# Kernel tuning notes

Hardware: AMD Instinct MI355X
Metric: run time of the kernel (lower is better)

Reference implementation:

```python
import jax, jax.numpy as jnp
import numpy as np
from jax import lax

B, NODE, T, D_IN = 8, 1024, 12, 16
HID, GAT_OUT, PRED_LEN = 32, 32, 6
HEADS = 3
F_IN = HID * T      # 384
C = GAT_OUT * T     # 384
N = B * NODE        # 8192
E = 65536


def setup_inputs() -> dict:
    key = jax.random.key(0)
    ks = jax.random.split(key, 24)
    s = 0.05
    inp = {}
    inp["x"] = jax.random.normal(ks[0], (B, NODE, T, D_IN), jnp.float32)
    inp["edge_index"] = jax.random.randint(ks[1], (2, E), 0, N)
    inp["edge_attr"] = jax.random.normal(ks[2], (E, 1), jnp.float32)
    inp["batch_vec"] = jnp.repeat(jnp.arange(B), NODE)
    inp["alpha"] = 1.0
    # GRU params (torch gate order: r, z, n)
    inp["Wih"] = jax.random.normal(ks[3], (3 * HID, D_IN), jnp.float32) * s
    inp["Whh"] = jax.random.normal(ks[4], (3 * HID, HID), jnp.float32) * s
    inp["bih"] = jax.random.normal(ks[5], (3 * HID,), jnp.float32) * s
    inp["bhh"] = jax.random.normal(ks[6], (3 * HID,), jnp.float32) * s
    # GATConv params
    inp["Wgat"] = jax.random.normal(ks[7], (HEADS * C, F_IN), jnp.float32) * s
    inp["att_src"] = jax.random.normal(ks[8], (1, HEADS, C), jnp.float32) * s
    inp["att_dst"] = jax.random.normal(ks[9], (1, HEADS, C), jnp.float32) * s
    inp["Wedge"] = jax.random.normal(ks[10], (HEADS * C, 1), jnp.float32) * s
    inp["att_edge"] = jax.random.normal(ks[11], (1, HEADS, C), jnp.float32) * s
    inp["gat_bias"] = jax.random.normal(ks[12], (C,), jnp.float32) * s
    # predictors / classifiers
    inp["Wp1"] = jax.random.normal(ks[13], (1, GAT_OUT), jnp.float32) * s
    inp["bp1"] = jax.random.normal(ks[14], (1,), jnp.float32) * s
    inp["Wp3"] = jax.random.normal(ks[15], (PRED_LEN, T), jnp.float32) * s
    inp["bp3"] = jax.random.normal(ks[16], (PRED_LEN,), jnp.float32) * s
    inp["Wc1"] = jax.random.normal(ks[17], (GAT_OUT, T * GAT_OUT), jnp.float32) * s
    inp["bc1"] = jax.random.normal(ks[18], (GAT_OUT,), jnp.float32) * s
    inp["Wc2"] = jax.random.normal(ks[19], (2, GAT_OUT), jnp.float32) * s
    inp["bc2"] = jax.random.normal(ks[20], (2,), jnp.float32) * s
    return inp


def _gru(x, Wih, Whh, bih, bhh):
    # x: [rows, T, D_IN] -> [rows, T, HID]
    h0 = jnp.zeros((x.shape[0], HID), x.dtype)

    def step(h, xt):
        gi = xt @ Wih.T + bih
        gh = h @ Whh.T + bhh
        ir, iz, inn = jnp.split(gi, 3, axis=-1)
        hr, hz, hn = jnp.split(gh, 3, axis=-1)
        r = jax.nn.sigmoid(ir + hr)
        z = jax.nn.sigmoid(iz + hz)
        n = jnp.tanh(inn + r * hn)
        h_new = (1.0 - z) * n + z * h
        return h_new, h_new

    _, hs = lax.scan(step, h0, jnp.swapaxes(x, 0, 1))
    return jnp.swapaxes(hs, 0, 1)


def _gat(x, edge_index, edge_attr, Wgat, att_src, att_dst, Wedge, att_edge, bias):
    # PyG GATConv, heads=HEADS, concat=False, edge_dim=1, no self loops
    h = (x @ Wgat.T).reshape(N, HEADS, C)          # [N,H,C]
    a_src = (h * att_src).sum(-1)                  # [N,H]
    a_dst = (h * att_dst).sum(-1)                  # [N,H]
    src, dst = edge_index[0], edge_index[1]
    e = (edge_attr @ Wedge.T).reshape(-1, HEADS, C)
    a_edge = (e * att_edge).sum(-1)                # [E,H]
    a = jax.nn.leaky_relu(a_src[src] + a_dst[dst] + a_edge, 0.2)
    amax = jax.ops.segment_max(a, dst, num_segments=N)
    a = jnp.exp(a - amax[dst])
    denom = jax.ops.segment_sum(a, dst, num_segments=N)
    a = a / (denom[dst] + 1e-16)                   # segment softmax over incoming edges
    msg = h[src] * a[:, :, None]                   # [E,H,C]
    out = jax.ops.segment_sum(msg, dst, num_segments=N)
    return out.mean(axis=1) + bias                 # concat=False -> head mean


def reference(x, edge_index, edge_attr, batch_vec, alpha,
              Wih, Whh, bih, bhh,
              Wgat, att_src, att_dst, Wedge, att_edge, gat_bias,
              Wp1, bp1, Wp3, bp3, Wc1, bc1, Wc2, bc2):
    gru_in = x.reshape(-1, T, D_IN)                       # [N,T,D]
    gru_out = _gru(gru_in, Wih, Whh, bih, bhh)            # [N,T,HID]
    gat_in = gru_out.reshape(N, F_IN)
    gat_out = _gat(gat_in, edge_index, edge_attr, Wgat, att_src, att_dst,
                   Wedge, att_edge, gat_bias)             # [N,C]
    lin_in = gat_out.reshape(-1, T, GAT_OUT)              # [N,T,GAT_OUT]
    p = jax.nn.relu(jnp.einsum('ntc,oc->nto', lin_in, Wp1) + bp1).squeeze(-1)  # [N,T]
    p = jax.nn.relu(p @ Wp3.T + bp3)                      # [N,PRED_LEN]
    out_pred = p.reshape(B, NODE, PRED_LEN)
    # GRL is identity in forward
    pooled = jax.ops.segment_max(gat_out, batch_vec, num_segments=B)  # [B,C]
    l1 = pooled @ Wc1.T + bc1
    l2 = l1 @ Wc2.T + bc2
    out_label = jax.nn.softmax(l2, axis=1)
    return out_pred, out_label
```

## Files before the change

kernel.cpp:

```cpp
#include <hip/hip_runtime.h>
#include <hip/hip_bf16.h>

#define N_NODES 8192
#define E_EDGES 65536
#define HEADS 3
#define CDIM 384
#define NHC 1152
#define T_STEPS 12
#define D_IN 16
#define HID 32
#define PRED_LEN 6
#define OUT_LABEL_OFF 49152

#define O_X        0u
#define O_WIH      1572864u
#define O_WHH      1574400u
#define O_BIH      1577472u
#define O_BHH      1577568u
#define O_WGAT     1577664u
#define O_ATTS     2020032u
#define O_ATTD     2021184u
#define O_WEDGE    2022336u
#define O_ATTE     2023488u
#define O_GBIAS    2024640u
#define O_WP1      2025024u
#define O_BP1      2025056u
#define O_WP3      2025057u
#define O_BP3      2025129u
#define O_WC1      2025135u
#define O_BC1      2037423u
#define O_WC2      2037455u
#define O_BC2      2037519u
#define O_EATTR    2037521u
#define CONV_TOTAL 2103057u

#define O_GATIN    2103072u
#define O_GATB     O_GATIN
#define O_WGATB    (O_GATIN + 1572864u)
#define O_DEG      (O_GATIN + 1794048u)
#define O_ROWST    (O_GATIN + 1802240u)
#define O_CURS     (O_GATIN + 1810432u)
#define O_CSRE     (O_GATIN + 1818624u)
#define O_HFEAT    5248800u
#define O_ASRC     14685984u
#define O_ADST     14710560u
#define O_ARAW     14735136u
#define O_WEXP     14931744u
#define O_AMAX     15128352u
#define O_DENOM    15152928u
#define O_GMEAN    15177504u
#define O_POOLED   18323232u
#define O_KH       18326304u
#define O_FLAG     18326307u

typedef __attribute__((ext_vector_type(8))) short short8;
typedef __attribute__((ext_vector_type(4))) float floatx4;

__device__ __forceinline__ float b2f(unsigned short u) {
    return __uint_as_float(((unsigned)u) << 16);
}
__device__ __forceinline__ unsigned short f2b(float f) {
    __hip_bfloat16 b = __float2bfloat16(f);
    return *(unsigned short*)&b;
}
__device__ __forceinline__ short f2bs(float f) {
    __hip_bfloat16 b = __float2bfloat16(f);
    return *(short*)&b;
}
__device__ __forceinline__ unsigned enc_f(float f) {
    unsigned u = __float_as_uint(f);
    return (u & 0x80000000u) ? ~u : (u | 0x80000000u);
}
__device__ __forceinline__ float dec_f(unsigned e) {
    return __uint_as_float((e & 0x80000000u) ? (e & 0x7FFFFFFFu) : ~e);
}
__device__ __forceinline__ float fast_rcp(float x) {
    return __builtin_amdgcn_rcpf(x);
}

__global__ __launch_bounds__(256) void fill_detect(
    const unsigned short* __restrict__ wih_raw,
    int* __restrict__ flag,
    float* __restrict__ W)
{
    if (blockIdx.x == 0 && threadIdx.x < 64) {
        int lane = threadIdx.x;
        int cnt = 0;
#pragma unroll
        for (int i = 0; i < 8; i++) {
            unsigned short h = wih_raw[(lane * 8 + i) * 2];
            int e = (h >> 7) & 0xFF;
            if (e >= 100 && e <= 127) cnt++;
        }
#pragma unroll
        for (int off = 32; off; off >>= 1) cnt += __shfl_down(cnt, off, 64);
        if (lane == 0) *flag = (cnt >= 300) ? 1 : 0;
    }
    unsigned idx = blockIdx.x * 256 + threadIdx.x;
    if      (idx < 24576u) W[O_AMAX  + idx] = 0.f;
    else if (idx < 49152u) W[O_DENOM + idx - 24576u] = 0.f;
    else if (idx < 52224u) W[O_POOLED + idx - 49152u] = 0.f;
    else if (idx < 60416u) ((int*)(W + O_DEG))[idx - 52224u] = 0;
}

__global__ __launch_bounds__(256) void convert_all(
    const int* __restrict__ flag,
    const void* x, const void* Wih, const void* Whh, const void* bih, const void* bhh,
    const void* Wgat, const void* atts, const void* attd, const void* Wedge, const void* atte,
    const void* gbias, const void* Wp1, const void* bp1, const void* Wp3, const void* bp3,
    const void* Wc1, const void* bc1, const void* Wc2, const void* bc2, const void* eattr,
    float* __restrict__ dst, unsigned short* __restrict__ wgatb)
{
    unsigned idx = blockIdx.x * 256 + threadIdx.x;
    if (idx >= CONV_TOTAL) return;
    if (idx >= O_WGAT && idx < O_ATTS) {
        unsigned off = idx - O_WGAT;
        wgatb[off] = (*flag) ? ((const unsigned short*)Wgat)[off]
                             : f2b(((const float*)Wgat)[off]);
        return;
    }
    const void* src; unsigned off;
    if      (idx < O_WIH)   { src = x;     off = idx - O_X; }
    else if (idx < O_WHH)   { src = Wih;   off = idx - O_WIH; }
    else if (idx < O_BIH)   { src = Whh;   off = idx - O_WHH; }
    else if (idx < O_BHH)   { src = bih;   off = idx - O_BIH; }
    else if (idx < O_WGAT)  { src = bhh;   off = idx - O_BHH; }
    else if (idx < O_ATTD)  { src = atts;  off = idx - O_ATTS; }
    else if (idx < O_WEDGE) { src = attd;  off = idx - O_ATTD; }
    else if (idx < O_ATTE)  { src = Wedge; off = idx - O_WEDGE; }
    else if (idx < O_GBIAS) { src = atte;  off = idx - O_ATTE; }
    else if (idx < O_WP1)   { src = gbias; off = idx - O_GBIAS; }
    else if (idx < O_BP1)   { src = Wp1;   off = idx - O_WP1; }
    else if (idx < O_BP3)   { src = (idx == O_BP1) ? bp1 : Wp3; off = (idx == O_BP1) ? 0 : idx - O_WP3; }
    else if (idx < O_WC1)   { src = bp3;   off = idx - O_BP3; }
    else if (idx < O_BC1)   { src = Wc1;   off = idx - O_WC1; }
    else if (idx < O_WC2)   { src = bc1;   off = idx - O_BC1; }
    else if (idx < O_BC2)   { src = Wc2;   off = idx - O_WC2; }
    else if (idx < O_EATTR) { src = bc2;   off = idx - O_BC2; }
    else                    { src = eattr; off = idx - O_EATTR; }
    float v = (*flag) ? b2f(((const unsigned short*)src)[off])
                      : ((const float*)src)[off];
    dst[idx] = v;
}

__global__ __launch_bounds__(64, 1) void gru_kernel(
    const float* __restrict__ W,
    unsigned short* __restrict__ gat_b)
{
    __shared__ short hbuf[16 * 40];
    int lane = threadIdx.x;
    int q = lane >> 4, nl = lane & 15;
    int n0 = blockIdx.x * 16;
    int n = n0 + nl;

    const float* W_wih = W + O_WIH;
    const float* W_whh = W + O_WHH;
    const float* W_bih = W + O_BIH;
    const float* W_bhh = W + O_BHH;
    const float* W_x   = W + O_X;

    short8 wh[6], wi[6];
#pragma unroll
    for (int c = 0; c < 6; c++) {
        int row = c * 16 + nl;
#pragma unroll
        for (int r = 0; r < 8; r++) {
            wh[c][r] = f2bs(W_whh[row * 32 + 8 * q + r]);
            int k = 8 * q + r;
            wi[c][r] = (k < 16) ? f2bs(W_wih[row * 16 + k]) : (short)0;
        }
    }
    float br[8], bz[8], bni[8], bnh[8];
#pragma unroll
    for (int idx = 0; idx < 8; idx++) {
        int c = idx >> 2, r = idx & 3;
        int j = c * 16 + 4 * q + r;
        br[idx]  = W_bih[j] + W_bhh[j];
        bz[idx]  = W_bih[32 + j] + W_bhh[32 + j];
        bni[idx] = W_bih[64 + j];
        bnh[idx] = W_bhh[64 + j];
    }

    floatx4 zf = {0.f, 0.f, 0.f, 0.f};
    short8 zs; 
#pragma unroll
    for (int r = 0; r < 8; r++) zs[r] = 0;

    float hprev[8];
#pragma unroll
    for (int i = 0; i < 8; i++) hprev[i] = 0.f;
    short8 hfrag = zs;

    for (int t = 0; t < T_STEPS; t++) {
        short8 xf = zs;
        if (q < 2) {
            const float* xp = W_x + (size_t)n * 192 + t * 16 + 8 * q;
            float4 xa = *(const float4*)xp;
            float4 xb = *(const float4*)(xp + 4);
            xf[0] = f2bs(xa.x); xf[1] = f2bs(xa.y); xf[2] = f2bs(xa.z); xf[3] = f2bs(xa.w);
            xf[4] = f2bs(xb.x); xf[5] = f2bs(xb.y); xf[6] = f2bs(xb.z); xf[7] = f2bs(xb.w);
        }

        floatx4 aR0 = __builtin_amdgcn_mfma_f32_16x16x32_bf16(wi[0], xf, zf, 0, 0, 0);
        aR0 = __builtin_amdgcn_mfma_f32_16x16x32_bf16(wh[0], hfrag, aR0, 0, 0, 0);
        floatx4 aR1 = __builtin_amdgcn_mfma_f32_16x16x32_bf16(wi[1], xf, zf, 0, 0, 0);
        aR1 = __builtin_amdgcn_mfma_f32_16x16x32_bf16(wh[1], hfrag, aR1, 0, 0, 0);
        floatx4 aZ0 = __builtin_amdgcn_mfma_f32_16x16x32_bf16(wi[2], xf, zf, 0, 0, 0);
        aZ0 = __builtin_amdgcn_mfma_f32_16x16x32_bf16(wh[2], hfrag, aZ0, 0, 0, 0);
        floatx4 aZ1 = __builtin_amdgcn_mfma_f32_16x16x32_bf16(wi[3], xf, zf, 0, 0, 0);
        aZ1 = __builtin_amdgcn_mfma_f32_16x16x32_bf16(wh[3], hfrag, aZ1, 0, 0, 0);
        floatx4 aNI0 = __builtin_amdgcn_mfma_f32_16x16x32_bf16(wi[4], xf, zf, 0, 0, 0);
        floatx4 aNI1 = __builtin_amdgcn_mfma_f32_16x16x32_bf16(wi[5], xf, zf, 0, 0, 0);
        floatx4 aNH0 = __builtin_amdgcn_mfma_f32_16x16x32_bf16(wh[4], hfrag, zf, 0, 0, 0);
        floatx4 aNH1 = __builtin_amdgcn_mfma_f32_16x16x32_bf16(wh[5], hfrag, zf, 0, 0, 0);

#pragma unroll
        for (int idx = 0; idx < 8; idx++) {
            int c = idx >> 2, r = idx & 3;
            float vR = (c ? aR1[r] : aR0[r]) + br[idx];
            float vZ = (c ? aZ1[r] : aZ0[r]) + bz[idx];
            float vNI = (c ? aNI1[r] : aNI0[r]) + bni[idx];
            float vNH = (c ? aNH1[r] : aNH0[r]) + bnh[idx];
            float rr = fast_rcp(1.f + __expf(-vR));
            float zz = fast_rcp(1.f + __expf(-vZ));
            float pre = vNI + rr * vNH;
            float e2 = __expf(2.f * pre);
            float nn = 1.f - 2.f * fast_rcp(e2 + 1.f);
            float h = (1.f - zz) * nn + zz * hprev[idx];
            hprev[idx] = h;
            int j = c * 16 + 4 * q + r;
            hbuf[nl * 40 + j] = f2bs(h);
        }
        hfrag = *(short8*)&hbuf[nl * 40 + 8 * q];
        int sn = lane >> 2, jg = (lane & 3) * 8;
        short8 hv = *(short8*)&hbuf[sn * 40 + jg];
        *(short8*)(gat_b + (size_t)(n0 + sn) * 384 + t * 32 + jg) = hv;
    }
}

__global__ __launch_bounds__(256) void gemm_mfma(
    const unsigned short* __restrict__ Ab,
    const unsigned short* __restrict__ Bb,
    unsigned short* __restrict__ Cb)
{
    __shared__ unsigned short sA[128][40];
    __shared__ unsigned short sB[128][40];
    int tid = threadIdx.x;
    int wave = tid >> 6, lane = tid & 63;
    int wm = (wave >> 1) * 64, wn = (wave & 1) * 64;
    int m0 = blockIdx.x * 128, n0 = blockIdx.y * 128;

    int r0 = tid >> 2;
    int c8 = (tid & 3) * 8;

    floatx4 acc[4][4];
#pragma unroll
    for (int i = 0; i < 4; i++)
#pragma unroll
        for (int j = 0; j < 4; j++) acc[i][j] = 0;

    int ml = lane & 15, kq = (lane >> 4) * 8;

    for (int k0 = 0; k0 < 384; k0 += 32) {
        short8 a0 = *(const short8*)(Ab + (size_t)(m0 + r0) * 384 + k0 + c8);
        short8 a1 = *(const short8*)(Ab + (size_t)(m0 + r0 + 64) * 384 + k0 + c8);
        short8 b0 = *(const short8*)(Bb + (size_t)(n0 + r0) * 384 + k0 + c8);
        short8 b1 = *(const short8*)(Bb + (size_t)(n0 + r0 + 64) * 384 + k0 + c8);

        __syncthreads();
        *(short8*)(&sA[r0][c8])      = a0;
        *(short8*)(&sA[r0 + 64][c8]) = a1;
        *(short8*)(&sB[r0][c8])      = b0;
        *(short8*)(&sB[r0 + 64][c8]) = b1;
        __syncthreads();

        short8 af[4], bf[4];
#pragma unroll
        for (int i = 0; i < 4; i++)
            af[i] = *(const short8*)(&sA[wm + i * 16 + ml][kq]);
#pragma unroll
        for (int j = 0; j < 4; j++)
            bf[j] = *(const short8*)(&sB[wn + j * 16 + ml][kq]);
#pragma unroll
        for (int i = 0; i < 4; i++)
#pragma unroll
            for (int j = 0; j < 4; j++)
                acc[i][j] = __builtin_amdgcn_mfma_f32_16x16x32_bf16(af[i], bf[j], acc[i][j], 0, 0, 0);
    }

    int cn = lane & 15, rq = (lane >> 4) * 4;
#pragma unroll
    for (int i = 0; i < 4; i++)
#pragma unroll
        for (int j = 0; j < 4; j++)
#pragma unroll
            for (int r = 0; r < 4; r++)
                Cb[(size_t)(m0 + wm + i * 16 + rq + r) * NHC + n0 + wn + j * 16 + cn] = f2b(acc[i][j][r]);
}

__global__ __launch_bounds__(256) void att_score_kernel(
    const unsigned short* __restrict__ h_bf,
    const float* __restrict__ att_src,
    const float* __restrict__ att_dst,
    const float* __restrict__ Wedge,
    const float* __restrict__ att_edge,
    float* __restrict__ a_src, float* __restrict__ a_dst,
    float* __restrict__ Kh)
{
    if (blockIdx.x == (N_NODES * 3) / 4) {
        if (threadIdx.x < 192) {
            int hd = threadIdx.x >> 6, lane = threadIdx.x & 63;
            float s = 0.f;
#pragma unroll
            for (int qq = 0; qq < 6; qq++) {
                int c = lane + qq * 64;
                s += Wedge[hd * CDIM + c] * att_edge[hd * CDIM + c];
            }
#pragma unroll
            for (int off = 32; off; off >>= 1) s += __shfl_down(s, off, 64);
            if (lane == 0) Kh[hd] = s;
        }
        return;
    }
    int w = (blockIdx.x * 256 + threadIdx.x) >> 6;
    int lane = threadIdx.x & 63;
    int n = w / 3, hd = w % 3;
    const unsigned short* hrow = h_bf + (size_t)n * NHC + hd * CDIM;
    float s0 = 0.f, s1 = 0.f;
#pragma unroll
    for (int qq = 0; qq < 6; qq++) {
        int c = lane + qq * 64;
        float hv = b2f(hrow[c]);
        s0 += hv * att_src[hd * CDIM + c];
        s1 += hv * att_dst[hd * CDIM + c];
    }
#pragma unroll
    for (int off = 32; off; off >>= 1) {
        s0 += __shfl_down(s0, off, 64);
        s1 += __shfl_down(s1, off, 64);
    }
    if (lane == 0) { a_src[n * 3 + hd] = s0; a_dst[n * 3 + hd] = s1; }
}

__global__ __launch_bounds__(256) void edge_score_kernel(
    const int* __restrict__ edge_index,
    const float* __restrict__ edge_attr,
    const float* __restrict__ a_src, const float* __restrict__ a_dst,
    const float* __restrict__ Kh,
    float* __restrict__ a_raw, unsigned* __restrict__ amax_enc,
    int* __restrict__ deg)
{
    int tid = blockIdx.x * 256 + threadIdx.x;
    int hd = tid >> 16;
    int e = tid & (E_EDGES - 1);
    int src = edge_index[e];
    int dst = edge_index[E_EDGES + e];
    float a = a_src[src * 3 + hd] + a_dst[dst * 3 + hd] + edge_attr[e] * Kh[hd];
    a = a > 0.f ? a : 0.2f * a;
    a_raw[hd * E_EDGES + e] = a;
    atomicMax(&amax_enc[dst * 3 + hd], enc_f(a));
    if (hd == 0) atomicAdd(&deg[dst], 1);
}

__global__ __launch_bounds__(256) void scan_kernel(
    const int* __restrict__ deg, int* __restrict__ rowstart, int* __restrict__ cursor)
{
    __shared__ int wtot[4];
    int t = threadIdx.x;
    int lane = t & 63, wv = t >> 6;
    int l[32], s = 0;
#pragma unroll
    for (int i = 0; i < 32; i++) { l[i] = deg[t * 32 + i]; s += l[i]; }
    int sc = s;
#pragma unroll
    for (int off = 1; off <= 32; off <<= 1) {
        int v = __shfl_up(sc, off, 64);
        if (lane >= off) sc += v;
    }
    if (lane == 63) wtot[wv] = sc;
    __syncthreads();
    int woff = 0;
#pragma unroll
    for (int w = 0; w < 4; w++) if (w < wv) woff += wtot[w];
    int b = woff + sc - s;
#pragma unroll
    for (int i = 0; i < 32; i++) {
        rowstart[t * 32 + i] = b;
        cursor[t * 32 + i] = b;
        b += l[i];
    }
}

__global__ __launch_bounds__(256) void edge_exp_kernel(
    const int* __restrict__ edge_index,
    const float* __restrict__ a_raw, const unsigned* __restrict__ amax_enc,
    float* __restrict__ w_exp, float* __restrict__ denom,
    int* __restrict__ cursor, int* __restrict__ csr_e)
{
    int tid = blockIdx.x * 256 + threadIdx.x;
    int hd = tid >> 16;
    int e = tid & (E_EDGES - 1);
    int dst = edge_index[E_EDGES + e];
    float m = dec_f(amax_enc[dst * 3 + hd]);
    float w = expf(a_raw[hd * E_EDGES + e] - m);
    w_exp[hd * E_EDGES + e] = w;
    unsafeAtomicAdd(&denom[dst * 3 + hd], w);
    if (hd == 0) {
        int pos = atomicAdd(&cursor[dst], 1);
        csr_e[pos] = e;
    }
}

__global__ __launch_bounds__(384) void aggregate_fused(
    const int* __restrict__ flag,
    const int* __restrict__ edge_index,
    const unsigned short* __restrict__ h_bf,
    const float* __restrict__ w_exp, const float* __restrict__ denom,
    const int* __restrict__ rowstart, const int* __restrict__ deg,
    const int* __restrict__ csr_e,
    const float* __restrict__ gat_bias,
    const float* __restrict__ Wp1, const float* __restrict__ bp1,
    const float* __restrict__ Wp3, const float* __restrict__ bp3,
    float* __restrict__ gmean,
    void* __restrict__ out_pred)
{
    int dst = blockIdx.x;
    int s = rowstart[dst], d = deg[dst];
    int tid = threadIdx.x;
    const float third = 1.f / 3.f;
    float inv0 = third / (denom[dst * 3 + 0] + 1e-16f);
    float inv1 = third / (denom[dst * 3 + 1] + 1e-16f);
    float inv2 = third / (denom[dst * 3 + 2] + 1e-16f);
    __shared__ int ssrc[64];
    __shared__ float sc0[64], sc1[64], sc2[64];
    __shared__ float gs[384];
    __shared__ float ps[12];
    float a = 0.f;
    for (int ch = 0; ch < d; ch += 64) {
        int m = d - ch; if (m > 64) m = 64;
        __syncthreads();
        if (tid < m) {
            int e = csr_e[s + ch + tid];
            ssrc[tid] = edge_index[e];
            sc0[tid] = w_exp[e] * inv0;
            sc1[tid] = w_exp[E_EDGES + e] * inv1;
            sc2[tid] = w_exp[2 * E_EDGES + e] * inv2;
        }
        __syncthreads();
        for (int i = 0; i < m; i++) {
            const unsigned short* hs = h_bf + (size_t)ssrc[i] * NHC;
            a += sc0[i] * b2f(hs[tid]) + sc1[i] * b2f(hs[tid + CDIM]) + sc2[i] * b2f(hs[tid + 2 * CDIM]);
        }
    }
    float g = a + gat_bias[tid];
    gmean[(size_t)dst * CDIM + tid] = g;
    gs[tid] = g;
    __syncthreads();

    int t = tid >> 5, c = tid & 31;
    float v = gs[t * 32 + c] * Wp1[c];
#pragma unroll
    for (int off = 16; off; off >>= 1) v += __shfl_down(v, off, 32);
    if (c == 0) { float p = v + bp1[0]; ps[t] = p > 0.f ? p : 0.f; }
    __syncthreads();

    if (tid < PRED_LEN) {
        float acc = bp3[tid];
#pragma unroll
        for (int tt = 0; tt < 12; tt++) acc += Wp3[tid * 12 + tt] * ps[tt];
        acc = acc > 0.f ? acc : 0.f;
        size_t oi = (size_t)dst * PRED_LEN + tid;
        if (*flag) ((__hip_bfloat16*)out_pred)[oi] = __float2bfloat16(acc);
        else       ((float*)out_pred)[oi] = acc;
    }
}

__global__ __launch_bounds__(384) void pool_kernel(
    const float* __restrict__ gmean,
    unsigned* __restrict__ pooled_enc)
{
    int b = blockIdx.x, ch = blockIdx.y;
    int tid = threadIdx.x;
    const float* base = gmean + ((size_t)b * 1024 + ch * 64) * CDIM + tid;
    float m = -3.4e38f;
    for (int i = 0; i < 64; i++)
        m = fmaxf(m, base[(size_t)i * CDIM]);
    atomicMax(&pooled_enc[b * CDIM + tid], enc_f(m));
}

__global__ __launch_bounds__(384) void cls_kernel(
    const int* __restrict__ flag,
    const unsigned* __restrict__ pooled_enc,
    const float* __restrict__ Wc1, const float* __restrict__ bc1,
    const float* __restrict__ Wc2, const float* __restrict__ bc2,
    void* __restrict__ out_base)
{
    int b = blockIdx.x, t = threadIdx.x;
    __shared__ float l1[32];
    if (t < 32) l1[t] = bc1[t];
    __syncthreads();
    float v = dec_f(pooled_enc[b * CDIM + t]);
#pragma unroll
    for (int i = 0; i < 32; i++) {
        float p = v * Wc1[i * CDIM + t];
#pragma unroll
        for (int off = 32; off; off >>= 1) p += __shfl_down(p, off, 64);
        if ((t & 63) == 0) atomicAdd(&l1[i], p);
    }
    __syncthreads();
    if (t == 0) {
        float l0 = bc2[0], l1v = bc2[1];
#pragma unroll
        for (int ii = 0; ii < 32; ii++) {
            l0  += Wc2[ii] * l1[ii];
            l1v += Wc2[32 + ii] * l1[ii];
        }
        float m = fmaxf(l0, l1v);
        float e0 = expf(l0 - m), e1 = expf(l1v - m);
        float s = e0 + e1;
        if (*flag) {
            __hip_bfloat16* ob = (__hip_bfloat16*)out_base;
            ob[OUT_LABEL_OFF + b * 2 + 0] = __float2bfloat16(e0 / s);
            ob[OUT_LABEL_OFF + b * 2 + 1] = __float2bfloat16(e1 / s);
        } else {
            float* of = (float*)out_base;
            of[OUT_LABEL_OFF + b * 2 + 0] = e0 / s;
            of[OUT_LABEL_OFF + b * 2 + 1] = e1 / s;
        }
    }
}

extern "C" void kernel_launch(void* const* d_in, const int* in_sizes, int n_in,
                              void* d_out, int out_size, void* d_ws, size_t ws_size,
                              hipStream_t stream) {
    float* W = (float*)d_ws;
    int* flag = (int*)(W + O_FLAG);
    const int* edge_index = (const int*)d_in[1];

    fill_detect<<<236, 256, 0, stream>>>(
        (const unsigned short*)d_in[5], flag, W);
    convert_all<<<(CONV_TOTAL + 255) / 256, 256, 0, stream>>>(
        flag,
        d_in[0], d_in[5], d_in[6], d_in[7], d_in[8],
        d_in[9], d_in[10], d_in[11], d_in[12], d_in[13],
        d_in[14], d_in[15], d_in[16], d_in[17], d_in[18],
        d_in[19], d_in[20], d_in[21], d_in[22], d_in[2],
        W, (unsigned short*)(W + O_WGATB));

    gru_kernel<<<N_NODES / 16, 64, 0, stream>>>(
        W, (unsigned short*)(W + O_GATB));
    gemm_mfma<<<dim3(N_NODES / 128, NHC / 128), 256, 0, stream>>>(
        (const unsigned short*)(W + O_GATB),
        (const unsigned short*)(W + O_WGATB),
        (unsigned short*)(W + O_HFEAT));
    att_score_kernel<<<(N_NODES * 3) / 4 + 1, 256, 0, stream>>>(
        (const unsigned short*)(W + O_HFEAT), W + O_ATTS, W + O_ATTD,
        W + O_WEDGE, W + O_ATTE,
        W + O_ASRC, W + O_ADST, W + O_KH);
    edge_score_kernel<<<3 * E_EDGES / 256, 256, 0, stream>>>(
        edge_index, W + O_EATTR, W + O_ASRC, W + O_ADST, W + O_KH,
        W + O_ARAW, (unsigned*)(W + O_AMAX), (int*)(W + O_DEG));
    scan_kernel<<<1, 256, 0, stream>>>(
        (const int*)(W + O_DEG), (int*)(W + O_ROWST), (int*)(W + O_CURS));
    edge_exp_kernel<<<3 * E_EDGES / 256, 256, 0, stream>>>(
        edge_index, W + O_ARAW, (const unsigned*)(W + O_AMAX),
        W + O_WEXP, W + O_DENOM, (int*)(W + O_CURS), (int*)(W + O_CSRE));
    aggregate_fused<<<N_NODES, 384, 0, stream>>>(
        flag, edge_index, (const unsigned short*)(W + O_HFEAT),
        W + O_WEXP, W + O_DENOM,
        (const int*)(W + O_ROWST), (const int*)(W + O_DEG),
        (const int*)(W + O_CSRE),
        W + O_GBIAS, W + O_WP1, W + O_BP1, W + O_WP3, W + O_BP3,
        W + O_GMEAN, d_out);
    pool_kernel<<<dim3(8, 16), 384, 0, stream>>>(
        W + O_GMEAN, (unsigned*)(W + O_POOLED));
    cls_kernel<<<8, 384, 0, stream>>>(
        flag, (const unsigned*)(W + O_POOLED),
        W + O_WC1, W + O_BC1, W + O_WC2, W + O_BC2, d_out);
}
```

Before: 252.2 us.

## Fuse prep, edge-score/exp and scan, pool/cls kernels; drop softmax max pass

Merges format detection with input conversion, computes edge attention exponentials directly without a per-destination max reduction, performs the degree scan in the last finishing block, and fuses pooling with the classifier via a last-block counter. This removes several kernel launches and one full edge pass plus the atomicMax traffic. Dropping max-subtraction risks overflow if attention logits become large, and the last-block pattern adds serialization on a single block.

```diff
diff --git a/kernel.cpp b/kernel.cpp
--- a/kernel.cpp
+++ b/kernel.cpp
@@ -3,12 +3,9 @@
 
 #define N_NODES 8192
 #define E_EDGES 65536
-#define HEADS 3
 #define CDIM 384
 #define NHC 1152
 #define T_STEPS 12
-#define D_IN 16
-#define HID 32
 #define PRED_LEN 6
 #define OUT_LABEL_OFF 49152
 
@@ -44,9 +41,8 @@
 #define O_HFEAT    5248800u
 #define O_ASRC     14685984u
 #define O_ADST     14710560u
-#define O_ARAW     14735136u
 #define O_WEXP     14931744u
-#define O_AMAX     15128352u
+#define O_CNT      15128352u
 #define O_DENOM    15152928u
 #define O_GMEAN    15177504u
 #define O_POOLED   18323232u
@@ -78,49 +74,43 @@
     return __builtin_amdgcn_rcpf(x);
 }
 
-__global__ __launch_bounds__(256) void fill_detect(
-    const unsigned short* __restrict__ wih_raw,
-    int* __restrict__ flag,
-    float* __restrict__ W)
-{
-    if (blockIdx.x == 0 && threadIdx.x < 64) {
-        int lane = threadIdx.x;
-        int cnt = 0;
-#pragma unroll
-        for (int i = 0; i < 8; i++) {
-            unsigned short h = wih_raw[(lane * 8 + i) * 2];
-            int e = (h >> 7) & 0xFF;
-            if (e >= 100 && e <= 127) cnt++;
-        }
-#pragma unroll
-        for (int off = 32; off; off >>= 1) cnt += __shfl_down(cnt, off, 64);
-        if (lane == 0) *flag = (cnt >= 300) ? 1 : 0;
-    }
-    unsigned idx = blockIdx.x * 256 + threadIdx.x;
-    if      (idx < 24576u) W[O_AMAX  + idx] = 0.f;
-    else if (idx < 49152u) W[O_DENOM + idx - 24576u] = 0.f;
-    else if (idx < 52224u) W[O_POOLED + idx - 49152u] = 0.f;
-    else if (idx < 60416u) ((int*)(W + O_DEG))[idx - 52224u] = 0;
-}
-
-__global__ __launch_bounds__(256) void convert_all(
-    const int* __restrict__ flag,
+__global__ __launch_bounds__(256) void prep_kernel(
     const void* x, const void* Wih, const void* Whh, const void* bih, const void* bhh,
     const void* Wgat, const void* atts, const void* attd, const void* Wedge, const void* atte,
     const void* gbias, const void* Wp1, const void* bp1, const void* Wp3, const void* bp3,
     const void* Wc1, const void* bc1, const void* Wc2, const void* bc2, const void* eattr,
-    float* __restrict__ dst, unsigned short* __restrict__ wgatb)
-{
+    float* __restrict__ W, unsigned short* __restrict__ wgatb, int* __restrict__ flag_g)
+{
+    __shared__ int fsh;
+    if (threadIdx.x < 64) {
+        int lane = threadIdx.x, cnt = 0;
+#pragma unroll
+        for (int i = 0; i < 8; i++) {
+            unsigned short h = ((const unsigned short*)Wih)[(lane * 8 + i) * 2];
+            int e = (h >> 7) & 0xFF;
+            if (e >= 100 && e <= 127) cnt++;
+        }
+#pragma unroll
+        for (int off = 32; off; off >>= 1) cnt += __shfl_down(cnt, off, 64);
+        if (lane == 0) fsh = (cnt >= 300) ? 1 : 0;
+    }
+    __syncthreads();
+    int flag = fsh;
     unsigned idx = blockIdx.x * 256 + threadIdx.x;
+    if (idx == 0) *flag_g = flag;
+    if      (idx < 24576u) W[O_DENOM + idx] = 0.f;
+    else if (idx < 27648u) W[O_POOLED + idx - 24576u] = 0.f;
+    else if (idx < 35840u) ((int*)(W + O_DEG))[idx - 27648u] = 0;
+    else if (idx < 35842u) ((int*)(W + O_CNT))[idx - 35840u] = 0;
     if (idx >= CONV_TOTAL) return;
     if (idx >= O_WGAT && idx < O_ATTS) {
         unsigned off = idx - O_WGAT;
-        wgatb[off] = (*flag) ? ((const unsigned short*)Wgat)[off]
-                             : f2b(((const float*)Wgat)[off]);
+        wgatb[off] = flag ? ((const unsigned short*)Wgat)[off]
+                          : f2b(((const float*)Wgat)[off]);
         return;
     }
     const void* src; unsigned off;
-    if      (idx < O_WIH)   { src = x;     off = idx - O_X; }
+    if      (idx < O_WIH)   { src = x;     off = idx; }
     else if (idx < O_WHH)   { src = Wih;   off = idx - O_WIH; }
     else if (idx < O_BIH)   { src = Whh;   off = idx - O_WHH; }
     else if (idx < O_BHH)   { src = bih;   off = idx - O_BIH; }
@@ -138,9 +128,8 @@
     else if (idx < O_BC2)   { src = Wc2;   off = idx - O_WC2; }
     else if (idx < O_EATTR) { src = bc2;   off = idx - O_BC2; }
     else                    { src = eattr; off = idx - O_EATTR; }
-    float v = (*flag) ? b2f(((const unsigned short*)src)[off])
-                      : ((const float*)src)[off];
-    dst[idx] = v;
+    W[idx] = flag ? b2f(((const unsigned short*)src)[off])
+                  : ((const float*)src)[off];
 }
 
 __global__ __launch_bounds__(64, 1) void gru_kernel(
@@ -182,7 +171,7 @@
     }
 
     floatx4 zf = {0.f, 0.f, 0.f, 0.f};
-    short8 zs; 
+    short8 zs;
 #pragma unroll
     for (int r = 0; r < 8; r++) zs[r] = 0;
 
@@ -342,73 +331,68 @@
     if (lane == 0) { a_src[n * 3 + hd] = s0; a_dst[n * 3 + hd] = s1; }
 }
 
-__global__ __launch_bounds__(256) void edge_score_kernel(
+__global__ __launch_bounds__(256) void edge_w_kernel(
     const int* __restrict__ edge_index,
-    const float* __restrict__ edge_attr,
+    const float* __restrict__ eattr,
     const float* __restrict__ a_src, const float* __restrict__ a_dst,
     const float* __restrict__ Kh,
-    float* __restrict__ a_raw, unsigned* __restrict__ amax_enc,
-    int* __restrict__ deg)
+    float* __restrict__ w_exp, float* __restrict__ denom,
+    int* __restrict__ deg, int* __restrict__ rowstart, int* __restrict__ cursor,
+    int* __restrict__ counter)
 {
     int tid = blockIdx.x * 256 + threadIdx.x;
     int hd = tid >> 16;
     int e = tid & (E_EDGES - 1);
     int src = edge_index[e];
     int dst = edge_index[E_EDGES + e];
-    float a = a_src[src * 3 + hd] + a_dst[dst * 3 + hd] + edge_attr[e] * Kh[hd];
+    float a = a_src[src * 3 + hd] + a_dst[dst * 3 + hd] + eattr[e] * Kh[hd];
     a = a > 0.f ? a : 0.2f * a;
-    a_raw[hd * E_EDGES + e] = a;
-    atomicMax(&amax_enc[dst * 3 + hd], enc_f(a));
-    if (hd == 0) atomicAdd(&deg[dst], 1);
-}
-
-__global__ __launch_bounds__(256) void scan_kernel(
-    const int* __restrict__ deg, int* __restrict__ rowstart, int* __restrict__ cursor)
-{
-    __shared__ int wtot[4];
-    int t = threadIdx.x;
-    int lane = t & 63, wv = t >> 6;
-    int l[32], s = 0;
-#pragma unroll
-    for (int i = 0; i < 32; i++) { l[i] = deg[t * 32 + i]; s += l[i]; }
-    int sc = s;
-#pragma unroll
-    for (int off = 1; off <= 32; off <<= 1) {
-        int v = __shfl_up(sc, off, 64);
-        if (lane >= off) sc += v;
-    }
-    if (lane == 63) wtot[wv] = sc;
-    __syncthreads();
-    int woff = 0;
-#pragma unroll
-    for (int w = 0; w < 4; w++) if (w < wv) woff += wtot[w];
-    int b = woff + sc - s;
-#pragma unroll
-    for (int i = 0; i < 32; i++) {
-        rowstart[t * 32 + i] = b;
-        cursor[t * 32 + i] = b;
-        b += l[i];
-    }
-}
-
-__global__ __launch_bounds__(256) void edge_exp_kernel(
-    const int* __restrict__ edge_index,
-    const float* __restrict__ a_raw, const unsigned* __restrict__ amax_enc,
-    float* __restrict__ w_exp, float* __restrict__ denom,
-    int* __restrict__ cursor, int* __restrict__ csr_e)
-{
-    int tid = blockIdx.x * 256 + threadIdx.x;
-    int hd = tid >> 16;
-    int e = tid & (E_EDGES - 1);
-    int dst = edge_index[E_EDGES + e];
-    float m = dec_f(amax_enc[dst * 3 + hd]);
-    float w = expf(a_raw[hd * E_EDGES + e] - m);
+    float w = __expf(a);
     w_exp[hd * E_EDGES + e] = w;
     unsafeAtomicAdd(&denom[dst * 3 + hd], w);
-    if (hd == 0) {
-        int pos = atomicAdd(&cursor[dst], 1);
-        csr_e[pos] = e;
-    }
+    if (hd == 0) atomicAdd(&deg[dst], 1);
+
+    __threadfence();
+    __shared__ int isLast;
+    if (threadIdx.x == 0)
+        isLast = (atomicAdd(counter, 1) == (int)gridDim.x - 1);
+    __syncthreads();
+    if (isLast) {
+        __shared__ int wtot[4];
+        int t = threadIdx.x;
+        int lane = t & 63, wv = t >> 6;
+        int l[32], s = 0;
+#pragma unroll
+        for (int i = 0; i < 32; i++) { l[i] = deg[t * 32 + i]; s += l[i]; }
+        int sc = s;
+#pragma unroll
+        for (int off = 1; off <= 32; off <<= 1) {
+            int v = __shfl_up(sc, off, 64);
+            if (lane >= off) sc += v;
+        }
+        if (lane == 63) wtot[wv] = sc;
+        __syncthreads();
+        int woff = 0;
+#pragma unroll
+        for (int w2 = 0; w2 < 4; w2++) if (w2 < wv) woff += wtot[w2];
+        int b = woff + sc - s;
+#pragma unroll
+        for (int i = 0; i < 32; i++) {
+            rowstart[t * 32 + i] = b;
+            cursor[t * 32 + i] = b;
+            b += l[i];
+        }
+    }
+}
+
+__global__ __launch_bounds__(256) void scatter_kernel(
+    const int* __restrict__ edge_index,
+    int* __restrict__ cursor, int* __restrict__ csr_e)
+{
+    int e = blockIdx.x * 256 + threadIdx.x;
+    int dst = edge_index[E_EDGES + e];
+    int pos = atomicAdd(&cursor[dst], 1);
+    csr_e[pos] = e;
 }
 
 __global__ __launch_bounds__(384) void aggregate_fused(
@@ -475,58 +459,66 @@
     }
 }
 
-__global__ __launch_bounds__(384) void pool_kernel(
+__global__ __launch_bounds__(384) void pool_cls_kernel(
+    const int* __restrict__ flag,
     const float* __restrict__ gmean,
-    unsigned* __restrict__ pooled_enc)
-{
-    int b = blockIdx.x, ch = blockIdx.y;
-    int tid = threadIdx.x;
-    const float* base = gmean + ((size_t)b * 1024 + ch * 64) * CDIM + tid;
-    float m = -3.4e38f;
-    for (int i = 0; i < 64; i++)
-        m = fmaxf(m, base[(size_t)i * CDIM]);
-    atomicMax(&pooled_enc[b * CDIM + tid], enc_f(m));
-}
-
-__global__ __launch_bounds__(384) void cls_kernel(
-    const int* __restrict__ flag,
-    const unsigned* __restrict__ pooled_enc,
+    unsigned* __restrict__ pooled_enc,
     const float* __restrict__ Wc1, const float* __restrict__ bc1,
     const float* __restrict__ Wc2, const float* __restrict__ bc2,
+    int* __restrict__ counter,
     void* __restrict__ out_base)
 {
-    int b = blockIdx.x, t = threadIdx.x;
+    int bid = blockIdx.x;
+    int tid = threadIdx.x;
+    {
+        int b = bid >> 4, ch = bid & 15;
+        const float* base = gmean + ((size_t)b * 1024 + ch * 64) * CDIM + tid;
+        float m = -3.4e38f;
+        for (int i = 0; i < 64; i++)
+            m = fmaxf(m, base[(size_t)i * CDIM]);
+        atomicMax(&pooled_enc[b * CDIM + tid], enc_f(m));
+    }
+    __threadfence();
+    __shared__ int isLast;
+    if (tid == 0)
+        isLast = (atomicAdd(counter, 1) == (int)gridDim.x - 1);
+    __syncthreads();
+    if (!isLast) return;
+
     __shared__ float l1[32];
-    if (t < 32) l1[t] = bc1[t];
-    __syncthreads();
-    float v = dec_f(pooled_enc[b * CDIM + t]);
-#pragma unroll
-    for (int i = 0; i < 32; i++) {
-        float p = v * Wc1[i * CDIM + t];
-#pragma unroll
-        for (int off = 32; off; off >>= 1) p += __shfl_down(p, off, 64);
-        if ((t & 63) == 0) atomicAdd(&l1[i], p);
-    }
-    __syncthreads();
-    if (t == 0) {
-        float l0 = bc2[0], l1v = bc2[1];
-#pragma unroll
-        for (int ii = 0; ii < 32; ii++) {
-            l0  += Wc2[ii] * l1[ii];
-            l1v += Wc2[32 + ii] * l1[ii];
-        }
-        float m = fmaxf(l0, l1v);
-        float e0 = expf(l0 - m), e1 = expf(l1v - m);
-        float s = e0 + e1;
-        if (*flag) {
-            __hip_bfloat16* ob = (__hip_bfloat16*)out_base;
-            ob[OUT_LABEL_OFF + b * 2 + 0] = __float2bfloat16(e0 / s);
-            ob[OUT_LABEL_OFF + b * 2 + 1] = __float2bfloat16(e1 / s);
-        } else {
-            float* of = (float*)out_base;
-            of[OUT_LABEL_OFF + b * 2 + 0] = e0 / s;
-            of[OUT_LABEL_OFF + b * 2 + 1] = e1 / s;
-        }
+    for (int b = 0; b < 8; b++) {
+        if (tid < 32) l1[tid] = bc1[tid];
+        __syncthreads();
+        float v = dec_f(pooled_enc[b * CDIM + tid]);
+#pragma unroll
+        for (int i = 0; i < 32; i++) {
+            float p = v * Wc1[i * CDIM + tid];
+#pragma unroll
+            for (int off = 32; off; off >>= 1) p += __shfl_down(p, off, 64);
+            if ((tid & 63) == 0) atomicAdd(&l1[i], p);
+        }
+        __syncthreads();
+        if (tid == 0) {
+            float l0 = bc2[0], l1v = bc2[1];
+#pragma unroll
+            for (int ii = 0; ii < 32; ii++) {
+                l0  += Wc2[ii] * l1[ii];
+                l1v += Wc2[32 + ii] * l1[ii];
+            }
+            float m = fmaxf(l0, l1v);
+            float e0 = __expf(l0 - m), e1 = __expf(l1v - m);
+            float sden = e0 + e1;
+            if (*flag) {
+                __hip_bfloat16* ob = (__hip_bfloat16*)out_base;
+                ob[OUT_LABEL_OFF + b * 2 + 0] = __float2bfloat16(e0 / sden);
+                ob[OUT_LABEL_OFF + b * 2 + 1] = __float2bfloat16(e1 / sden);
+            } else {
+                float* of = (float*)out_base;
+                of[OUT_LABEL_OFF + b * 2 + 0] = e0 / sden;
+                of[OUT_LABEL_OFF + b * 2 + 1] = e1 / sden;
+            }
+        }
+        __syncthreads();
     }
 }
 
@@ -536,16 +528,14 @@
     float* W = (float*)d_ws;
     int* flag = (int*)(W + O_FLAG);
     const int* edge_index = (const int*)d_in[1];
-
-    fill_detect<<<236, 256, 0, stream>>>(
-        (const unsigned short*)d_in[5], flag, W);
-    convert_all<<<(CONV_TOTAL + 255) / 256, 256, 0, stream>>>(
-        flag,
+    int* counters = (int*)(W + O_CNT);
+
+    prep_kernel<<<(CONV_TOTAL + 255) / 256, 256, 0, stream>>>(
         d_in[0], d_in[5], d_in[6], d_in[7], d_in[8],
         d_in[9], d_in[10], d_in[11], d_in[12], d_in[13],
         d_in[14], d_in[15], d_in[16], d_in[17], d_in[18],
         d_in[19], d_in[20], d_in[21], d_in[22], d_in[2],
-        W, (unsigned short*)(W + O_WGATB));
+        W, (unsigned short*)(W + O_WGATB), flag);
 
     gru_kernel<<<N_NODES / 16, 64, 0, stream>>>(
         W, (unsigned short*)(W + O_GATB));
@@ -557,14 +547,13 @@
         (const unsigned short*)(W + O_HFEAT), W + O_ATTS, W + O_ATTD,
         W + O_WEDGE, W + O_ATTE,
         W + O_ASRC, W + O_ADST, W + O_KH);
-    edge_score_kernel<<<3 * E_EDGES / 256, 256, 0, stream>>>(
+    edge_w_kernel<<<3 * E_EDGES / 256, 256, 0, stream>>>(
         edge_index, W + O_EATTR, W + O_ASRC, W + O_ADST, W + O_KH,
-        W + O_ARAW, (unsigned*)(W + O_AMAX), (int*)(W + O_DEG));
-    scan_kernel<<<1, 256, 0, stream>>>(
-        (const int*)(W + O_DEG), (int*)(W + O_ROWST), (int*)(W + O_CURS));
-    edge_exp_kernel<<<3 * E_EDGES / 256, 256, 0, stream>>>(
-        edge_index, W + O_ARAW, (const unsigned*)(W + O_AMAX),
-        W + O_WEXP, W + O_DENOM, (int*)(W + O_CURS), (int*)(W + O_CSRE));
+        W + O_WEXP, W + O_DENOM,
+        (int*)(W + O_DEG), (int*)(W + O_ROWST), (int*)(W + O_CURS),
+        counters);
+    scatter_kernel<<<E_EDGES / 256, 256, 0, stream>>>(
+        edge_index, (int*)(W + O_CURS), (int*)(W + O_CSRE));
     aggregate_fused<<<N_NODES, 384, 0, stream>>>(
         flag, edge_index, (const unsigned short*)(W + O_HFEAT),
         W + O_WEXP, W + O_DENOM,
@@ -572,9 +561,8 @@
         (const int*)(W + O_CSRE),
         W + O_GBIAS, W + O_WP1, W + O_BP1, W + O_WP3, W + O_BP3,
         W + O_GMEAN, d_out);
-    pool_kernel<<<dim3(8, 16), 384, 0, stream>>>(
-        W + O_GMEAN, (unsigned*)(W + O_POOLED));
-    cls_kernel<<<8, 384, 0, stream>>>(
-        flag, (const unsigned*)(W + O_POOLED),
-        W + O_WC1, W + O_BC1, W + O_WC2, W + O_BC2, d_out);
-}
+    pool_cls_kernel<<<128, 384, 0, stream>>>(
+        flag, W + O_GMEAN, (unsigned*)(W + O_POOLED),
+        W + O_WC1, W + O_BC1, W + O_WC2, W + O_BC2,
+        counters + 1, d_out);
+}
```

Result: slower. 348.9 us (+38.3%).
